# Performance work log

Measured on AMD Instinct MI355X. Metric: run time of the kernel, lower is better.

## Reference

```python
import jax, jax.numpy as jnp
import numpy as np

BIG = 1e10


def _cylinder_query(radius, hmin, hmax, nsample, xyz, new_xyz, rot):
    # xyz: (B,N,3), new_xyz: (B,P,3), rot: (B,P,3,3) -> idx: (B,P,nsample) int32
    diff = xyz[:, None, :, :] - new_xyz[:, :, None, :]          # (B,P,N,3)
    local = jnp.einsum('bpnc,bpcd->bpnd', diff, rot)            # (B,P,N,3)
    x, y, z = local[..., 0], local[..., 1], local[..., 2]
    r2 = y * y + z * z                                          # (B,P,N)
    in_cyl = (x >= hmin) & (x <= hmax) & (r2 < radius * radius)
    dist = jnp.where(in_cyl, r2, BIG)
    neg_vals, idx = jax.lax.top_k(-dist, nsample)               # smallest dists
    vals = -neg_vals
    valid = vals < 1e9
    first = idx[:, :, 0:1]
    idx = jnp.where(valid, idx, first)                          # (B,P,nsample)
    return idx


def _group(features, idx):
    # features: (B,C,N), idx: (B,P,S) -> (B,C,P,S)
    B, C, N = features.shape
    P, S = idx.shape[1], idx.shape[2]
    ft = jnp.swapaxes(features, 1, 2)                           # (B,N,C)
    flat = idx.reshape(B, P * S)
    out = jnp.take_along_axis(ft, flat[:, :, None], axis=1)     # (B,P*S,C)
    return jnp.transpose(out.reshape(B, P, S, C), (0, 3, 1, 2)) # (B,C,P,S)


def setup_inputs() -> dict:
    key = jax.random.key(0)
    k1, k2, k3, k4 = jax.random.split(key, 4)
    B, N, P, C = 4, 16384, 1024, 64
    xyz = jax.random.uniform(k1, (B, N, 3), dtype=jnp.float32)
    new_xyz = jax.random.uniform(k2, (B, P, 3), dtype=jnp.float32)
    rot = jax.random.normal(k3, (B, P, 3, 3), dtype=jnp.float32)
    features = jax.random.normal(k4, (B, C, N), dtype=jnp.float32)
    return {"radius": 0.3, "hmin": -0.02, "hmax": 0.04, "nsample": 32,
            "xyz": xyz, "new_xyz": new_xyz, "rot": rot, "features": features}


def reference(radius, hmin, hmax, nsample, xyz, new_xyz, rot, features):
    idx = _cylinder_query(radius, hmin, hmax, nsample, xyz, new_xyz, rot)
    xyz_t = jnp.swapaxes(xyz, 1, 2)                             # (B,3,N)
    grouped_xyz = _group(xyz_t, idx)                            # (B,3,P,S)
    grouped_xyz = grouped_xyz - jnp.swapaxes(new_xyz, 1, 2)[..., None]
    # rotate_xyz=True: (B,P,S,3) @ (B,P,3,3)
    g = jnp.transpose(grouped_xyz, (0, 2, 3, 1))
    g = jnp.einsum('bpsc,bpcd->bpsd', g, rot)
    grouped_xyz = jnp.transpose(g, (0, 3, 1, 2))                # (B,3,P,S)
    grouped_features = _group(features, idx)                    # (B,C,P,S)
    return jnp.concatenate([grouped_xyz, grouped_features], axis=1)
```

## Files before the change

kernel.cpp:

```cpp
#include <hip/hip_runtime.h>

#define CAP    4096
#define BIGK   1.0e300
#define IDXINF 0x7fffffff

__device__ __forceinline__ void cmpx(double& k, int& n, int lane, int stride, bool up) {
    double ok = __shfl_xor(k, stride);
    int    on = __shfl_xor(n, stride);
    bool oLess = (ok < k) || (ok == k && on < n);
    bool lower = (lane & stride) == 0;
    bool takeOther = lower ? (up ? oLess : !oLess) : (up ? !oLess : oLess);
    if (takeOther) { k = ok; n = on; }
}

__device__ __forceinline__ void wave_sort64(double& k, int& n, int lane, bool asc) {
    #pragma unroll
    for (int size = 2; size < 64; size <<= 1) {
        bool up = asc ? ((lane & size) == 0) : ((lane & size) != 0);
        #pragma unroll
        for (int stride = size >> 1; stride > 0; stride >>= 1)
            cmpx(k, n, lane, stride, up);
    }
    #pragma unroll
    for (int stride = 32; stride > 0; stride >>= 1)
        cmpx(k, n, lane, stride, asc);
}

__global__ __launch_bounds__(256) void cylgroup_kernel(
    const float* __restrict__ radius_p,
    const float* __restrict__ hmin_p,
    const float* __restrict__ hmax_p,
    const float* __restrict__ xyz,
    const float* __restrict__ new_xyz,
    const float* __restrict__ rot,
    const float* __restrict__ feat,
    float* __restrict__ out)
{
    const int N = 16384, P = 1024, C = 64, S = 32, OC = 3 + C;
    const int bp  = blockIdx.x;
    const int b   = bp >> 10;
    const int p   = bp & (P - 1);
    const int tid = threadIdx.x;
    const int lane = tid & 63;
    const int wv   = tid >> 6;

    __shared__ int    cn[CAP];
    __shared__ double wr2[256];
    __shared__ int    wn[256];
    __shared__ int    cnt;
    __shared__ int    sel[32];

    if (tid == 0) cnt = 0;
    __syncthreads();

    const double radius = (double)radius_p[0];
    const double hmin   = (double)hmin_p[0];
    const double hmax   = (double)hmax_p[0];
    const double rad2   = radius * radius;

    const float* nx = new_xyz + (size_t)bp * 3;
    const double cx = nx[0], cy = nx[1], cz = nx[2];
    const float* rp = rot + (size_t)bp * 9;
    const double r00 = rp[0], r01 = rp[1], r02 = rp[2];
    const double r10 = rp[3], r11 = rp[4], r12 = rp[5];
    const double r20 = rp[6], r21 = rp[7], r22 = rp[8];

    const float cxf = (float)cx, cyf = (float)cy, czf = (float)cz;
    const float r00f = (float)r00, r01f = (float)r01, r02f = (float)r02;
    const float r10f = (float)r10, r11f = (float)r11, r12f = (float)r12;
    const float r20f = (float)r20, r21f = (float)r21, r22f = (float)r22;
    const float hminf = (float)hmin - 1.0e-3f;
    const float hmaxf = (float)hmax + 1.0e-3f;
    const float rad2f = (float)rad2 + 1.0e-2f;

    const float* xb = xyz + (size_t)b * N * 3;

    auto exact_r2 = [&](int n) -> double {
        double dx = (double)xb[n * 3 + 0] - cx;
        double dy = (double)xb[n * 3 + 1] - cy;
        double dz = (double)xb[n * 3 + 2] - cz;
        double y = dx * r01 + dy * r11 + dz * r21;
        double z = dx * r02 + dy * r12 + dz * r22;
        return y * y + z * z;
    };

    for (int it = 0; it < 16; ++it) {
        int g = it * 1024 + tid * 4;
        const float4* vp = reinterpret_cast<const float4*>(xb + (size_t)g * 3);
        float4 v0 = vp[0], v1 = vp[1], v2 = vp[2];
        float px[4], py[4], pz[4];
        px[0]=v0.x; py[0]=v0.y; pz[0]=v0.z;
        px[1]=v0.w; py[1]=v1.x; pz[1]=v1.y;
        px[2]=v1.z; py[2]=v1.w; pz[2]=v2.x;
        px[3]=v2.y; py[3]=v2.z; pz[3]=v2.w;
        #pragma unroll
        for (int k = 0; k < 4; ++k) {
            float dxf = px[k] - cxf, dyf = py[k] - cyf, dzf = pz[k] - czf;
            float xf  = fmaf(dxf, r00f, fmaf(dyf, r10f, dzf * r20f));
            float yf  = fmaf(dxf, r01f, fmaf(dyf, r11f, dzf * r21f));
            float zf  = fmaf(dxf, r02f, fmaf(dyf, r12f, dzf * r22f));
            float r2f = fmaf(yf, yf, zf * zf);
            if (xf >= hminf && xf <= hmaxf && r2f < rad2f) {
                double dx = (double)px[k] - cx;
                double dy = (double)py[k] - cy;
                double dz = (double)pz[k] - cz;
                double x = dx * r00 + dy * r10 + dz * r20;
                double y = dx * r01 + dy * r11 + dz * r21;
                double z = dx * r02 + dy * r12 + dz * r22;
                double r2 = y * y + z * z;
                if (x >= hmin && x <= hmax && r2 < rad2) {
                    int slot = atomicAdd(&cnt, 1);
                    if (slot < CAP) cn[slot] = g + k;
                }
            }
        }
    }
    __syncthreads();

    const int M = min(cnt, CAP);

    double rk = BIGK; int rn = IDXINF;
    const int nch = (M + 63) >> 6;
    for (int ch = wv; ch < nch; ch += 4) {
        int j = (ch << 6) + lane;
        double ck; int cnn;
        if (j < M) { cnn = cn[j]; ck = exact_r2(cnn); }
        else       { ck = BIGK;   cnn = IDXINF; }
        wave_sort64(ck, cnn, lane, false);
        if ((ck < rk) || (ck == rk && cnn < rn)) { rk = ck; rn = cnn; }
        #pragma unroll
        for (int stride = 32; stride > 0; stride >>= 1)
            cmpx(rk, rn, lane, stride, true);
    }
    wr2[(wv << 6) + lane] = rk;
    wn [(wv << 6) + lane] = rn;
    __syncthreads();

    if (wv == 0) {
        #pragma unroll
        for (int w = 1; w < 4; ++w) {
            int src = (w << 6) + (63 - lane);
            double ck = wr2[src]; int cnn = wn[src];
            if ((ck < rk) || (ck == rk && cnn < rn)) { rk = ck; rn = cnn; }
            #pragma unroll
            for (int stride = 32; stride > 0; stride >>= 1)
                cmpx(rk, rn, lane, stride, true);
        }
        int nsel  = min(M, S);
        int first = __shfl(rn, 0);
        int v = (lane < nsel) ? rn : ((nsel > 0) ? first : 0);
        if (lane < S) sel[lane] = v;
    }
    __syncthreads();

    if (tid < S) {
        int n = sel[tid];
        double dx = (double)xb[n * 3 + 0] - cx;
        double dy = (double)xb[n * 3 + 1] - cy;
        double dz = (double)xb[n * 3 + 2] - cz;
        float x = (float)(dx * r00 + dy * r10 + dz * r20);
        float y = (float)(dx * r01 + dy * r11 + dz * r21);
        float z = (float)(dx * r02 + dy * r12 + dz * r22);
        float* o = out + (((size_t)b * OC + 0) * P + p) * S + tid;
        o[0 * (size_t)P * S] = x;
        o[1 * (size_t)P * S] = y;
        o[2 * (size_t)P * S] = z;
    }

    const float* fb = feat + (size_t)b * C * N;
    float* ob = out + (((size_t)b * OC + 3) * P + p) * S;
    for (int e = tid; e < C * S; e += 256) {
        int c = e >> 5;
        int s = e & 31;
        ob[(size_t)c * P * S + s] = fb[(size_t)c * N + sel[s]];
    }
}

extern "C" void kernel_launch(void* const* d_in, const int* in_sizes, int n_in,
                              void* d_out, int out_size, void* d_ws, size_t ws_size,
                              hipStream_t stream) {
    const float* radius  = (const float*)d_in[0];
    const float* hmin    = (const float*)d_in[1];
    const float* hmax    = (const float*)d_in[2];
    const float* xyz     = (const float*)d_in[4];
    const float* new_xyz = (const float*)d_in[5];
    const float* rot     = (const float*)d_in[6];
    const float* feat    = (const float*)d_in[7];
    float* out = (float*)d_out;

    dim3 grid(4096);
    dim3 block(256);
    hipLaunchKernelGGL(cylgroup_kernel, grid, block, 0, stream,
                       radius, hmin, hmax, xyz, new_xyz, rot, feat, out);
}
```

Baseline: 125.3 us.

## Split feature gather into separate channel-major kernel using 16-bit index workspace

Moves the per-point feature gather out of the selection kernel into a second kernel. That kernel stages one batch-half's selected indices (stored as 16-bit values in the workspace) into shared memory, then gathers one feature channel row per block, so reads come from a single 64 KB row and writes are contiguous. Candidate indices in shared memory also shrink to 16 bits. This adds a second launch and a workspace round trip, and splits occupancy between the two phases.

```diff
diff --git a/kernel.cpp b/kernel.cpp
--- a/kernel.cpp
+++ b/kernel.cpp
@@ -26,17 +26,17 @@
         cmpx(k, n, lane, stride, asc);
 }
 
-__global__ __launch_bounds__(256) void cylgroup_kernel(
+__global__ __launch_bounds__(256) void select_kernel(
     const float* __restrict__ radius_p,
     const float* __restrict__ hmin_p,
     const float* __restrict__ hmax_p,
     const float* __restrict__ xyz,
     const float* __restrict__ new_xyz,
     const float* __restrict__ rot,
-    const float* __restrict__ feat,
-    float* __restrict__ out)
+    float* __restrict__ out,
+    unsigned short* __restrict__ selw)
 {
-    const int N = 16384, P = 1024, C = 64, S = 32, OC = 3 + C;
+    const int N = 16384, P = 1024, S = 32, OC = 67;
     const int bp  = blockIdx.x;
     const int b   = bp >> 10;
     const int p   = bp & (P - 1);
@@ -44,7 +44,7 @@
     const int lane = tid & 63;
     const int wv   = tid >> 6;
 
-    __shared__ int    cn[CAP];
+    __shared__ unsigned short cn[CAP];
     __shared__ double wr2[256];
     __shared__ int    wn[256];
     __shared__ int    cnt;
@@ -110,7 +110,7 @@
                 double r2 = y * y + z * z;
                 if (x >= hmin && x <= hmax && r2 < rad2) {
                     int slot = atomicAdd(&cnt, 1);
-                    if (slot < CAP) cn[slot] = g + k;
+                    if (slot < CAP) cn[slot] = (unsigned short)(g + k);
                 }
             }
         }
@@ -155,6 +155,7 @@
 
     if (tid < S) {
         int n = sel[tid];
+        selw[(size_t)bp * S + tid] = (unsigned short)n;
         double dx = (double)xb[n * 3 + 0] - cx;
         double dy = (double)xb[n * 3 + 1] - cy;
         double dz = (double)xb[n * 3 + 2] - cz;
@@ -166,13 +167,36 @@
         o[1 * (size_t)P * S] = y;
         o[2 * (size_t)P * S] = z;
     }
-
-    const float* fb = feat + (size_t)b * C * N;
-    float* ob = out + (((size_t)b * OC + 3) * P + p) * S;
-    for (int e = tid; e < C * S; e += 256) {
-        int c = e >> 5;
-        int s = e & 31;
-        ob[(size_t)c * P * S + s] = fb[(size_t)c * N + sel[s]];
+}
+
+__global__ __launch_bounds__(256) void gather_kernel(
+    const float* __restrict__ feat,
+    const unsigned short* __restrict__ selw,
+    float* __restrict__ out)
+{
+    const int N = 16384, P = 1024, C = 64, S = 32, OC = 67;
+    const int bid  = blockIdx.x;
+    const int c    = bid & 63;
+    const int half = (bid >> 6) & 1;
+    const int b    = bid >> 7;
+    const int tid  = threadIdx.x;
+
+    __shared__ unsigned short st[512 * 32];
+
+    const uint4* sp = reinterpret_cast<const uint4*>(
+        selw + ((size_t)b * P + half * 512) * S);
+    uint4* dl = reinterpret_cast<uint4*>(st);
+    #pragma unroll
+    for (int k = 0; k < 8; ++k)
+        dl[k * 256 + tid] = sp[k * 256 + tid];
+    __syncthreads();
+
+    const float* fr = feat + ((size_t)b * C + c) * N;
+    float* ob = out + (((size_t)b * OC + 3 + c) * P + half * 512) * S;
+    #pragma unroll 4
+    for (int k = 0; k < 64; ++k) {
+        int e = k * 256 + tid;
+        ob[e] = fr[st[e]];
     }
 }
 
@@ -187,9 +211,10 @@
     const float* rot     = (const float*)d_in[6];
     const float* feat    = (const float*)d_in[7];
     float* out = (float*)d_out;
-
-    dim3 grid(4096);
-    dim3 block(256);
-    hipLaunchKernelGGL(cylgroup_kernel, grid, block, 0, stream,
-                       radius, hmin, hmax, xyz, new_xyz, rot, feat, out);
-}
+    unsigned short* selw = (unsigned short*)d_ws;
+
+    hipLaunchKernelGGL(select_kernel, dim3(4096), dim3(256), 0, stream,
+                       radius, hmin, hmax, xyz, new_xyz, rot, out, selw);
+    hipLaunchKernelGGL(gather_kernel, dim3(512), dim3(256), 0, stream,
+                       feat, selw, out);
+}
```

New measurement: 125.2 us. About the same (-0.2%).
